# Kernel tuning notes

Measured on AMD Instinct MI355X. Metric: run time of the kernel, lower is better.

## Reference

```python
import jax, jax.numpy as jnp
import numpy as np

D = 1024        # d_model
H = 16          # n_heads
DF = 4096       # d_ff
MAXL = 1024     # max_len
MAXSTEPS = 24   # max_steps


def setup_inputs() -> dict:
    key = jax.random.key(0)
    ks = jax.random.split(key, 10)
    B, S = 4, 1024
    s = 0.02
    f32 = jnp.float32
    return {
        "x": jax.random.normal(ks[0], (B, S, D), f32),
        "original_input": jax.random.normal(ks[1], (B, S, D), f32),
        "think_step": 5,
        "step_embed": jax.random.normal(ks[2], (MAXSTEPS, D), f32) * s,
        "Wqkv": jax.random.normal(ks[3], (D, 3 * D), f32) * s,
        "bqkv": jnp.zeros((3 * D,), f32),
        "Wout": jax.random.normal(ks[4], (D, D), f32) * s,
        "bout": jnp.zeros((D,), f32),
        "Wg": jax.random.normal(ks[5], (2 * D, D), f32) * s,
        "bg": jnp.zeros((D,), f32),
        "rel_pos_bias": jax.random.normal(ks[6], (2 * MAXL - 1,), f32) * s,
        "W1": jax.random.normal(ks[7], (D, DF), f32) * s,
        "b1": jnp.zeros((DF,), f32),
        "W2": jax.random.normal(ks[8], (DF, D), f32) * s,
        "b2": jnp.zeros((D,), f32),
        "ln1_g": jnp.ones((D,), f32),
        "ln1_b": jnp.zeros((D,), f32),
        "ln2_g": jnp.ones((D,), f32),
        "ln2_b": jnp.zeros((D,), f32),
    }


def _layer_norm(x, g, b, eps=1e-5):
    m = jnp.mean(x, axis=-1, keepdims=True)
    v = jnp.mean((x - m) ** 2, axis=-1, keepdims=True)
    return (x - m) * jax.lax.rsqrt(v + eps) * g + b


def reference(x, original_input, think_step, step_embed, Wqkv, bqkv, Wout, bout,
              Wg, bg, rel_pos_bias, W1, b1, W2, b2, ln1_g, ln1_b, ln2_g, ln2_b):
    B, S, _ = x.shape
    hd = D // H
    # gated residual input injection
    gate = jax.nn.sigmoid(jnp.concatenate([x, original_input], axis=-1) @ Wg + bg)
    x = x * (1.0 - gate) + original_input * gate
    # think-step embedding (clamped)
    step = min(int(think_step), MAXSTEPS - 1)
    x = x + step_embed[step][None, None, :]
    # qkv projection -> (3, B, H, S, hd)
    qkv = (x @ Wqkv + bqkv).reshape(B, S, 3, H, hd).transpose(2, 0, 3, 1, 4)
    q, k, v = qkv[0], qkv[1], qkv[2]
    scores = jnp.einsum('bhqd,bhkd->bhqk', q, k) * (hd ** -0.5)
    # relative position bias: dist clamped to [0, 2*MAXL-2]
    pos = jnp.arange(S)
    rel = jnp.clip(pos[:, None] - pos[None, :] + (MAXL - 1), 0, 2 * MAXL - 2)
    scores = scores + rel_pos_bias[rel][None, None]  # (B,H,S,S)
    probs = jax.nn.softmax(scores, axis=-1)
    attn = jnp.einsum('bhqk,bhkd->bhqd', probs, v)
    attn = attn.transpose(0, 2, 1, 3).reshape(B, S, D)
    attn = attn @ Wout + bout
    x = _layer_norm(x + attn, ln1_g, ln1_b)
    h = jax.nn.gelu(x @ W1 + b1, approximate=False) @ W2 + b2
    return _layer_norm(x + h, ln2_g, ln2_b)
```

## Files before the change

kernel.cpp:

```cpp
#include <hip/hip_runtime.h>
#include <hip/hip_bf16.h>
#include <math.h>

#define D_MODEL 1024
#define NH      16
#define HD      64
#define DFF     4096
#define SEQ     1024
#define BATCH   4
#define TOK     (BATCH*SEQ)
#define MAXSTEPS 24

typedef __hip_bfloat16 bf16;
typedef __attribute__((ext_vector_type(8))) short short8;
typedef __attribute__((ext_vector_type(4))) float floatx4;

__device__ __forceinline__ float b2f(bf16 v){ return __bfloat162float(v); }
__device__ __forceinline__ bf16  f2b(float v){ return __float2bfloat16(v); }

__device__ __forceinline__ void gload_lds16(const bf16* g, bf16* l){
    __builtin_amdgcn_global_load_lds((const __attribute__((address_space(1))) void*)g,
                                     (__attribute__((address_space(3))) void*)l, 16, 0, 0);
}

template<int TN, int EPI, bool SPLITK>
__global__ __launch_bounds__(256)
void mfma_gemm(const bf16* __restrict__ A, const bf16* __restrict__ Bt,
               const float* __restrict__ bias, void* __restrict__ outv,
               void* __restrict__ outv2,
               int M, int N, int K, int lda, int ldb,
               const float* __restrict__ xg, const float* __restrict__ og,
               const float* __restrict__ seg, const int* __restrict__ stepp)
{
    constexpr int NT  = TN / 32;
    constexpr int NBP = TN / 64;
    constexpr int R   = (TN == 64) ? 4 : 3;
    __shared__ bf16 As[R][128 * 32];
    __shared__ bf16 Bs[R][TN * 32];
    const int tid  = threadIdx.x;
    const int lane = tid & 63;
    const int w    = tid >> 6;
    const int wm   = w & 1, wn = w >> 1;
    const int fr   = lane & 15;
    const int q    = lane >> 4;

    if (SPLITK) {
        int z = blockIdx.z;
        A  += (size_t)z * K;
        Bt += (size_t)z * K;
    }

    const int tn_g = gridDim.x;
    const int nwg  = tn_g * gridDim.y;
    const int bid  = blockIdx.y * tn_g + blockIdx.x;
    const int o    = (bid & 7) * (nwg >> 3) + (bid >> 3);
    const int bandw = 8 * tn_g;
    const int band  = o / bandw;
    const int rr    = o - band * bandw;
    const int row0 = (band * 8 + (rr & 7)) * 128;
    const int col0 = (rr >> 3) * TN;

    const bf16* gA[2]; int sA_[2];
    #pragma unroll
    for (int p = 0; p < 2; ++p) {
        int s  = p * 256 + tid;
        int m  = s >> 2;
        int qg = (s & 3) ^ ((m >> 1) & 3);
        gA[p]  = A + (size_t)(row0 + m) * lda + qg * 8;
        sA_[p] = s * 8;
    }
    const bf16* gB[NBP]; int sB_[NBP];
    #pragma unroll
    for (int p = 0; p < NBP; ++p) {
        int s  = p * 256 + tid;
        int m  = s >> 2;
        int qg = (s & 3) ^ ((m >> 1) & 3);
        gB[p]  = Bt + (size_t)(col0 + m) * ldb + qg * 8;
        sB_[p] = s * 8;
    }

    int aoff[4], boff[NT];
    #pragma unroll
    for (int t = 0; t < 4; ++t) {
        int ml  = wm * 64 + t * 16 + fr;
        aoff[t] = (ml * 4 + (q ^ ((ml >> 1) & 3))) * 8;
    }
    #pragma unroll
    for (int t = 0; t < NT; ++t) {
        int nl  = wn * (TN / 2) + t * 16 + fr;
        boff[t] = (nl * 4 + (q ^ ((nl >> 1) & 3))) * 8;
    }

    #pragma unroll
    for (int pt = 0; pt < R - 1; ++pt) {
        #pragma unroll
        for (int p = 0; p < 2; ++p)   gload_lds16(gA[p] + pt * 32, &As[pt][sA_[p]]);
        #pragma unroll
        for (int p = 0; p < NBP; ++p) gload_lds16(gB[p] + pt * 32, &Bs[pt][sB_[p]]);
    }

    floatx4 acc[4][NT] = {};
    const int nk = K >> 5;
    int cur = 0;
    int kst = (R - 1) * 32;

    for (int t = 0; t < nk; ++t) {
        if constexpr (TN == 64) asm volatile("s_waitcnt vmcnt(6)" ::: "memory");
        else                    asm volatile("s_waitcnt vmcnt(4)" ::: "memory");
        __builtin_amdgcn_s_barrier();
        asm volatile("" ::: "memory");

        if (kst < K) {
            int sb = (cur == 0) ? (R - 1) : (cur - 1);
            #pragma unroll
            for (int p = 0; p < 2; ++p)   gload_lds16(gA[p] + kst, &As[sb][sA_[p]]);
            #pragma unroll
            for (int p = 0; p < NBP; ++p) gload_lds16(gB[p] + kst, &Bs[sb][sB_[p]]);
            kst += 32;
        }

        short8 af[4], bfg[NT];
        #pragma unroll
        for (int i = 0; i < 4; ++i)  af[i]  = *(const short8*)(&As[cur][aoff[i]]);
        #pragma unroll
        for (int j = 0; j < NT; ++j) bfg[j] = *(const short8*)(&Bs[cur][boff[j]]);
        #pragma unroll
        for (int i = 0; i < 4; ++i)
            #pragma unroll
            for (int j = 0; j < NT; ++j)
                acc[i][j] = __builtin_amdgcn_mfma_f32_16x16x32_bf16(af[i], bfg[j], acc[i][j], 0, 0, 0);

        cur = (cur == R - 1) ? 0 : (cur + 1);
    }

    void* outp = outv;
    float bscale = 1.0f;
    if (SPLITK && blockIdx.z != 0) { outp = outv2; bscale = 0.0f; }

    int st = 0;
    if (EPI == 3) {
        st = stepp[0];
        st = st < 0 ? 0 : (st > MAXSTEPS - 1 ? MAXSTEPS - 1 : st);
    }

    float bv[NT], sv[NT];
    #pragma unroll
    for (int nt = 0; nt < NT; ++nt) {
        int col = col0 + wn * (TN / 2) + nt * 16 + fr;
        bv[nt] = bias[col] * bscale;
        if (EPI == 3) sv[nt] = seg[st * D_MODEL + col];
    }
    #pragma unroll
    for (int mt = 0; mt < 4; ++mt) {
        #pragma unroll
        for (int nt = 0; nt < NT; ++nt) {
            int col = col0 + wn * (TN / 2) + nt * 16 + fr;
            #pragma unroll
            for (int r = 0; r < 4; ++r) {
                int row = row0 + wm * 64 + mt * 16 + q * 4 + r;
                float v = acc[mt][nt][r] + bv[nt];
                if (EPI == 0) {
                    ((float*)outp)[(size_t)row * N + col] = v;
                } else if (EPI == 1) {
                    ((bf16*)outp)[(size_t)row * N + col] = f2b(v);
                } else {
                    float g = 1.0f / (1.0f + __expf(-v));
                    size_t idx = (size_t)row * N + col;
                    float mix = xg[idx] * (1.0f - g) + og[idx] * g + sv[nt];
                    ((bf16*)outp)[idx] = f2b(mix);
                }
            }
        }
    }
}

template<int EPI>
__global__ __launch_bounds__(256, 2)
void gemm_wide(const bf16* __restrict__ A, const bf16* __restrict__ Bt,
               const float* __restrict__ bias, bf16* __restrict__ out,
               int M, int N, int K)
{
    constexpr int R = 3;
    __shared__ bf16 As[R][256 * 32];
    __shared__ bf16 Bs[R][128 * 32];
    const int tid  = threadIdx.x;
    const int lane = tid & 63;
    const int w    = tid >> 6;
    const int wm   = w & 1, wn = w >> 1;
    const int fr   = lane & 15;
    const int q    = lane >> 4;

    const int tn_g = gridDim.x;
    const int nwg  = tn_g * gridDim.y;
    const int bid  = blockIdx.y * tn_g + blockIdx.x;
    const int o    = (bid & 7) * (nwg >> 3) + (bid >> 3);
    const int bandw = 8 * tn_g;
    const int band  = o / bandw;
    const int rr    = o - band * bandw;
    const int row0 = (band * 8 + (rr & 7)) * 256;
    const int col0 = (rr >> 3) * 128;

    const bf16* gA[4]; int sA_[4];
    #pragma unroll
    for (int p = 0; p < 4; ++p) {
        int s  = p * 256 + tid;
        int m  = s >> 2;
        int qg = (s & 3) ^ ((m >> 1) & 3);
        gA[p]  = A + (size_t)(row0 + m) * K + qg * 8;
        sA_[p] = s * 8;
    }
    const bf16* gB[2]; int sB_[2];
    #pragma unroll
    for (int p = 0; p < 2; ++p) {
        int s  = p * 256 + tid;
        int m  = s >> 2;
        int qg = (s & 3) ^ ((m >> 1) & 3);
        gB[p]  = Bt + (size_t)(col0 + m) * K + qg * 8;
        sB_[p] = s * 8;
    }

    int aoff[8], boff[4];
    #pragma unroll
    for (int t = 0; t < 8; ++t) {
        int ml  = wm * 128 + t * 16 + fr;
        aoff[t] = (ml * 4 + (q ^ ((ml >> 1) & 3))) * 8;
    }
    #pragma unroll
    for (int t = 0; t < 4; ++t) {
        int nl  = wn * 64 + t * 16 + fr;
        boff[t] = (nl * 4 + (q ^ ((nl >> 1) & 3))) * 8;
    }

    #pragma unroll
    for (int pt = 0; pt < R - 1; ++pt) {
        #pragma unroll
        for (int p = 0; p < 4; ++p) gload_lds16(gA[p] + pt * 32, &As[pt][sA_[p]]);
        #pragma unroll
        for (int p = 0; p < 2; ++p) gload_lds16(gB[p] + pt * 32, &Bs[pt][sB_[p]]);
    }

    floatx4 acc[8][4] = {};
    const int nk = K >> 5;
    int cur = 0;
    int kst = (R - 1) * 32;

    for (int t = 0; t < nk; ++t) {
        asm volatile("s_waitcnt vmcnt(6)" ::: "memory");
        __builtin_amdgcn_s_barrier();
        asm volatile("" ::: "memory");

        if (kst < K) {
            int sb = (cur == 0) ? (R - 1) : (cur - 1);
            #pragma unroll
            for (int p = 0; p < 4; ++p) gload_lds16(gA[p] + kst, &As[sb][sA_[p]]);
            #pragma unroll
            for (int p = 0; p < 2; ++p) gload_lds16(gB[p] + kst, &Bs[sb][sB_[p]]);
            kst += 32;
        }

        short8 af[8], bfg[4];
        #pragma unroll
        for (int i = 0; i < 8; ++i) af[i]  = *(const short8*)(&As[cur][aoff[i]]);
        #pragma unroll
        for (int j = 0; j < 4; ++j) bfg[j] = *(const short8*)(&Bs[cur][boff[j]]);
        __builtin_amdgcn_s_setprio(1);
        #pragma unroll
        for (int i = 0; i < 8; ++i)
            #pragma unroll
            for (int j = 0; j < 4; ++j)
                acc[i][j] = __builtin_amdgcn_mfma_f32_16x16x32_bf16(af[i], bfg[j], acc[i][j], 0, 0, 0);
        __builtin_amdgcn_s_setprio(0);

        cur = (cur == R - 1) ? 0 : (cur + 1);
    }

    float bv[4];
    #pragma unroll
    for (int j = 0; j < 4; ++j) bv[j] = bias[col0 + wn * 64 + j * 16 + fr];
    #pragma unroll
    for (int mt = 0; mt < 8; ++mt) {
        #pragma unroll
        for (int nt = 0; nt < 4; ++nt) {
            int col = col0 + wn * 64 + nt * 16 + fr;
            #pragma unroll
            for (int r = 0; r < 4; ++r) {
                int row = row0 + wm * 128 + mt * 16 + q * 4 + r;
                float v = acc[mt][nt][r] + bv[nt];
                if (EPI == 1) {
                    out[(size_t)row * N + col] = f2b(v);
                } else {
                    float g = 0.5f * v * (1.0f + erff(v * 0.70710678118654752f));
                    out[(size_t)row * N + col] = f2b(g);
                }
            }
        }
    }
}

#define NTRANS_BLOCKS 14336
__global__ __launch_bounds__(256)
void transpose_all_kernel(const float* __restrict__ Wg,   bf16* __restrict__ WgT,
                          const float* __restrict__ Wqkv, bf16* __restrict__ WqkvT,
                          const float* __restrict__ Wout, bf16* __restrict__ WoutT,
                          const float* __restrict__ W1,   bf16* __restrict__ W1T,
                          const float* __restrict__ W2,   bf16* __restrict__ W2T)
{
    __shared__ float t[32][33];
    const int bid = blockIdx.x;
    if (bid >= NTRANS_BLOCKS) return;
    const float* W; bf16* WT; int K, N, base;
    if      (bid <  2048) { W = Wg;   WT = WgT;   K = 2048; N = 1024; base = 0; }
    else if (bid <  5120) { W = Wqkv; WT = WqkvT; K = 1024; N = 3072; base = 2048; }
    else if (bid <  6144) { W = Wout; WT = WoutT; K = 1024; N = 1024; base = 5120; }
    else if (bid < 10240) { W = W1;   WT = W1T;   K = 1024; N = 4096; base = 6144; }
    else                  { W = W2;   WT = W2T;   K = 4096; N = 1024; base = 10240; }
    const int lb  = bid - base;
    const int ntx = N >> 5;
    const int n0 = (lb % ntx) * 32, k0 = (lb / ntx) * 32;
    const int tx = threadIdx.x & 31, ty = threadIdx.x >> 5;
    #pragma unroll
    for (int i = 0; i < 4; ++i)
        t[ty + i * 8][tx] = W[(size_t)(k0 + ty + i * 8) * N + n0 + tx];
    __syncthreads();
    #pragma unroll
    for (int i = 0; i < 4; ++i)
        WT[(size_t)(n0 + ty + i * 8) * K + k0 + tx] = f2b(t[tx][ty + i * 8]);
}

__global__ __launch_bounds__(256)
void xcat_kernel(const float* __restrict__ x, const float* __restrict__ orig,
                 bf16* __restrict__ xcat)
{
    int i = blockIdx.x * 256 + threadIdx.x;
    float4 xv = ((const float4*)x)[i];
    float4 ov = ((const float4*)orig)[i];
    int t = i >> 8, c4 = (i & 255) * 4;
    bf16* px = xcat + (size_t)t * 2048 + c4;
    px[0] = f2b(xv.x); px[1] = f2b(xv.y); px[2] = f2b(xv.z); px[3] = f2b(xv.w);
    bf16* po = px + 1024;
    po[0] = f2b(ov.x); po[1] = f2b(ov.y); po[2] = f2b(ov.z); po[3] = f2b(ov.w);
}

__global__ __launch_bounds__(256)
void vtrans_kernel(const bf16* __restrict__ qkv, bf16* __restrict__ Vt)
{
    __shared__ float t[32][33];
    const int blk = blockIdx.x;
    const int dt = blk & 1;
    const int st = (blk >> 1) & 31;
    const int h  = (blk >> 6) & 15;
    const int b  = blk >> 10;
    const int tx = threadIdx.x & 31, ty = threadIdx.x >> 5;
    #pragma unroll
    for (int i = 0; i < 4; ++i)
        t[ty + i * 8][tx] = b2f(qkv[(size_t)(b * SEQ + st * 32 + ty + i * 8) * 3072
                                    + 2048 + h * 64 + dt * 32 + tx]);
    __syncthreads();
    #pragma unroll
    for (int i = 0; i < 4; ++i)
        Vt[(size_t)((b * NH + h) * 64 + dt * 32 + ty + i * 8) * SEQ + st * 32 + tx]
            = f2b(t[tx][ty + i * 8]);
}

__global__ __launch_bounds__(256)
void fattn_kernel(const bf16* __restrict__ qkv, const bf16* __restrict__ Vt,
                  const float* __restrict__ relb, bf16* __restrict__ out)
{
    __shared__ bf16 KPs[128 * 64];
    __shared__ bf16 Vs [64 * 128];
    __shared__ float relb_s[1088];

    const int tid  = threadIdx.x;
    const int lane = tid & 63;
    const int w    = tid >> 6;
    const int fr   = lane & 15;
    const int quad = lane >> 4;

    const int qt = blockIdx.x & 15;
    const int h  = (blockIdx.x >> 4) & 15;
    const int b  = blockIdx.x >> 8;
    const int bq = b * SEQ;
    const int bh = b * NH + h;

    for (int i = tid; i < 1087; i += 256)
        relb_s[i] = relb[qt * 64 + i] - 8.0f;

    const int qrow = bq + qt * 64 + w * 16 + fr;
    short8 qf[2];
    {
        const bf16* qp = qkv + (size_t)qrow * 3072 + h * 64 + quad * 8;
        qf[0] = *(const short8*)(qp);
        qf[1] = *(const short8*)(qp + 32);
    }

    int ibase[4];
    #pragma unroll
    for (int r = 0; r < 4; ++r)
        ibase[r] = (w * 16 + quad * 4 + r) - fr + 1023;

    float lsum[4] = {0.f, 0.f, 0.f, 0.f};
    floatx4 accO[4];
    #pragma unroll
    for (int nt = 0; nt < 4; ++nt) accO[nt] = (floatx4){0.f, 0.f, 0.f, 0.f};

    for (int k0 = 0; k0 < SEQ; k0 += 128) {
        __syncthreads();
        #pragma unroll
        for (int it = 0; it < 4; ++it) {
            int s = it * 256 + tid;
            int key = s >> 3, cs = s & 7;
            int c = cs ^ (key & 7);
            const bf16* src = qkv + (size_t)(bq + k0 + key) * 3072 + 1024 + h * 64 + c * 8;
            gload_lds16(src, KPs + (size_t)s * 8);
        }
        #pragma unroll
        for (int it = 0; it < 4; ++it) {
            int s = it * 256 + tid;
            int row = s >> 4, cs = s & 15;
            int c = cs ^ (row & 15);
            const bf16* src = Vt + (size_t)(bh * 64 + row) * SEQ + k0 + c * 8;
            gload_lds16(src, Vs + (size_t)s * 8);
        }
        __syncthreads();

        floatx4 accS[8];
        #pragma unroll
        for (int t = 0; t < 8; ++t) accS[t] = (floatx4){0.f, 0.f, 0.f, 0.f};
        __builtin_amdgcn_s_setprio(1);
        #pragma unroll
        for (int t = 0; t < 8; ++t) {
            int row = t * 16 + fr;
            #pragma unroll
            for (int ks = 0; ks < 2; ++ks) {
                int slot = (ks * 4 + quad) ^ (row & 7);
                short8 kf = *(const short8*)(KPs + (size_t)row * 64 + slot * 8);
                accS[t] = __builtin_amdgcn_mfma_f32_16x16x32_bf16(qf[ks], kf, accS[t], 0, 0, 0);
            }
        }
        __builtin_amdgcn_s_setprio(0);

        __syncthreads();

        bf16* Ps = KPs + w * 2048;
        #pragma unroll
        for (int t = 0; t < 8; ++t) {
            int keyl = t * 16 + fr;
            int cbase = keyl >> 3, koff = keyl & 7;
            #pragma unroll
            for (int r = 0; r < 4; ++r) {
                float bias = relb_s[ibase[r] - k0 - t * 16];
                float p = __expf(fmaf(accS[t][r], 0.125f, bias));
                lsum[r] += p;
                int row = quad * 4 + r;
                int slot = cbase ^ (row & 15);
                Ps[(size_t)row * 128 + slot * 8 + koff] = f2b(p);
            }
        }

        __builtin_amdgcn_s_setprio(1);
        #pragma unroll
        for (int ks = 0; ks < 4; ++ks) {
            int slotp = (ks * 4 + quad) ^ (fr & 15);
            short8 pf = *(const short8*)(Ps + (size_t)fr * 128 + slotp * 8);
            #pragma unroll
            for (int nt = 0; nt < 4; ++nt) {
                int vrow = nt * 16 + fr;
                int slotv = (ks * 4 + quad) ^ (vrow & 15);
                short8 vf = *(const short8*)(Vs + (size_t)vrow * 128 + slotv * 8);
                accO[nt] = __builtin_amdgcn_mfma_f32_16x16x32_bf16(pf, vf, accO[nt], 0, 0, 0);
            }
        }
        __builtin_amdgcn_s_setprio(0);
    }

    float inv[4];
    #pragma unroll
    for (int r = 0; r < 4; ++r) {
        float v = lsum[r];
        v += __shfl_xor(v, 1); v += __shfl_xor(v, 2);
        v += __shfl_xor(v, 4); v += __shfl_xor(v, 8);
        inv[r] = 1.0f / v;
    }

    #pragma unroll
    for (int nt = 0; nt < 4; ++nt) {
        int col = h * 64 + nt * 16 + fr;
        #pragma unroll
        for (int r = 0; r < 4; ++r) {
            int t = bq + qt * 64 + w * 16 + quad * 4 + r;
            out[(size_t)t * D_MODEL + col] = f2b(accO[nt][r] * inv[r]);
        }
    }
}

template<bool OUT_BF16, bool HAS2>
__global__ __launch_bounds__(256)
void ln_kernel(const bf16* __restrict__ a, const float* __restrict__ add,
               const float* __restrict__ add2,
               const float* __restrict__ g, const float* __restrict__ bb,
               void* __restrict__ outv)
{
    __shared__ float red[256];
    __shared__ float red2[256];
    const int row = blockIdx.x;
    const int tid = threadIdx.x;
    float s[4];
    float lsum = 0.f, lsq = 0.f;
    #pragma unroll
    for (int u = 0; u < 4; ++u) {
        int i = tid + 256 * u;
        float v = b2f(a[row * D_MODEL + i]) + add[row * D_MODEL + i];
        if (HAS2) v += add2[row * D_MODEL + i];
        s[u] = v; lsum += v; lsq += v * v;
    }
    red[tid] = lsum; red2[tid] = lsq; __syncthreads();
    for (int s2 = 128; s2 > 0; s2 >>= 1) {
        if (tid < s2) { red[tid] += red[tid + s2]; red2[tid] += red2[tid + s2]; }
        __syncthreads();
    }
    float mean = red[0] * (1.0f / D_MODEL);
    float var  = red2[0] * (1.0f / D_MODEL) - mean * mean;
    float rs = rsqrtf(var + 1e-5f);
    #pragma unroll
    for (int u = 0; u < 4; ++u) {
        int i = tid + 256 * u;
        float o = (s[u] - mean) * rs * g[i] + bb[i];
        if (OUT_BF16) ((bf16*)outv)[row * D_MODEL + i] = f2b(o);
        else          ((float*)outv)[row * D_MODEL + i] = o;
    }
}

extern "C" void kernel_launch(void* const* d_in, const int* in_sizes, int n_in,
                              void* d_out, int out_size, void* d_ws, size_t ws_size,
                              hipStream_t stream)
{
    const float* x     = (const float*)d_in[0];
    const float* orig  = (const float*)d_in[1];
    const int*   step  = (const int*)  d_in[2];
    const float* se    = (const float*)d_in[3];
    const float* Wqkv  = (const float*)d_in[4];
    const float* bqkv  = (const float*)d_in[5];
    const float* Wout  = (const float*)d_in[6];
    const float* bout  = (const float*)d_in[7];
    const float* Wg    = (const float*)d_in[8];
    const float* bg    = (const float*)d_in[9];
    const float* relb  = (const float*)d_in[10];
    const float* W1    = (const float*)d_in[11];
    const float* b1    = (const float*)d_in[12];
    const float* W2    = (const float*)d_in[13];
    const float* b2    = (const float*)d_in[14];
    const float* ln1g  = (const float*)d_in[15];
    const float* ln1b  = (const float*)d_in[16];
    const float* ln2g  = (const float*)d_in[17];
    const float* ln2b  = (const float*)d_in[18];

    char* ws = (char*)d_ws;
    bf16* WgT   = (bf16*)(ws);
    bf16* WqkvT = (bf16*)(ws + ( 4u << 20));
    bf16* WoutT = (bf16*)(ws + (10u << 20));
    bf16* W1T   = (bf16*)(ws + (12u << 20));
    bf16* W2T   = (bf16*)(ws + (20u << 20));
    bf16* xw    = (bf16*)(ws + (28u << 20));
    bf16* xcat  = (bf16*)(ws + (36u << 20));
    bf16* attnb = (bf16*)(ws + (36u << 20));
    bf16* h     = (bf16*)(ws + (44u << 20));
    bf16* qkvb  = (bf16*)(ws + (52u << 20));
    float* tmp2 = (float*)(ws);
    bf16* Vt    = (bf16*)d_out;
    float* tmp  = (float*)d_out;

    dim3 blk(256);

    transpose_all_kernel<<<NTRANS_BLOCKS, blk, 0, stream>>>(Wg, WgT, Wqkv, WqkvT,
                                                    Wout, WoutT, W1, W1T, W2, W2T);
    xcat_kernel<<<TOK, blk, 0, stream>>>(x, orig, xcat);

    mfma_gemm<64, 3, false><<<dim3(D_MODEL/64, TOK/128), blk, 0, stream>>>(
        xcat, WgT, bg, xw, nullptr, TOK, D_MODEL, 2*D_MODEL, 2*D_MODEL, 2*D_MODEL,
        x, orig, se, step);

    gemm_wide<1><<<dim3(3*D_MODEL/128, TOK/256), blk, 0, stream>>>(
        xw, WqkvT, bqkv, qkvb, TOK, 3*D_MODEL, D_MODEL);

    vtrans_kernel<<<BATCH*NH*64, blk, 0, stream>>>(qkvb, Vt);

    fattn_kernel<<<BATCH*NH*(SEQ/64), blk, 0, stream>>>(qkvb, Vt, relb, attnb);

    mfma_gemm<64, 0, false><<<dim3(D_MODEL/64, TOK/128), blk, 0, stream>>>(
        attnb, WoutT, bout, tmp, nullptr, TOK, D_MODEL, D_MODEL, D_MODEL, D_MODEL,
        nullptr, nullptr, nullptr, nullptr);

    ln_kernel<true, false><<<TOK, blk, 0, stream>>>(xw, tmp, nullptr, ln1g, ln1b, xw);

    gemm_wide<2><<<dim3(DFF/128, TOK/256), blk, 0, stream>>>(
        xw, W1T, b1, h, TOK, DFF, D_MODEL);

    mfma_gemm<128, 0, true><<<dim3(D_MODEL/128, TOK/128, 2), blk, 0, stream>>>(
        h, W2T, b2, tmp, tmp2, TOK, D_MODEL, DFF/2, DFF, DFF,
        nullptr, nullptr, nullptr, nullptr);

    ln_kernel<false, true><<<TOK, blk, 0, stream>>>(xw, tmp, tmp2, ln2g, ln2b, d_out);
}
```

Measured before the change: 432.0 us.

## Load A fragments directly into registers in wide GEMM, keep B in LDS

The wide GEMM used for QKV and FFN1 no longer stages the A tile through LDS. Each wave loads its A fragments straight from global memory into registers, double-buffered across two k-steps, while B stays in a triple-buffered LDS ring. This cuts LDS traffic and footprint and removes the A LDS reads. In exchange, A is fetched redundantly by the waves that share a row block, and register pressure rises, with global-load latency exposed more directly to the MFMA loop.

```diff
diff --git a/kernel.cpp b/kernel.cpp
--- a/kernel.cpp
+++ b/kernel.cpp
@@ -176,13 +176,11 @@
 
 template<int EPI>
 __global__ __launch_bounds__(256, 2)
-void gemm_wide(const bf16* __restrict__ A, const bf16* __restrict__ Bt,
+void gemm_areg(const bf16* __restrict__ A, const bf16* __restrict__ Bt,
                const float* __restrict__ bias, bf16* __restrict__ out,
                int M, int N, int K)
 {
-    constexpr int R = 3;
-    __shared__ bf16 As[R][256 * 32];
-    __shared__ bf16 Bs[R][128 * 32];
+    __shared__ bf16 Bs[3][128 * 32];
     const int tid  = threadIdx.x;
     const int lane = tid & 63;
     const int w    = tid >> 6;
@@ -200,15 +198,11 @@
     const int row0 = (band * 8 + (rr & 7)) * 256;
     const int col0 = (rr >> 3) * 128;
 
-    const bf16* gA[4]; int sA_[4];
-    #pragma unroll
-    for (int p = 0; p < 4; ++p) {
-        int s  = p * 256 + tid;
-        int m  = s >> 2;
-        int qg = (s & 3) ^ ((m >> 1) & 3);
-        gA[p]  = A + (size_t)(row0 + m) * K + qg * 8;
-        sA_[p] = s * 8;
-    }
+    const bf16* gAf[8];
+    #pragma unroll
+    for (int i = 0; i < 8; ++i)
+        gAf[i] = A + (size_t)(row0 + wm * 128 + i * 16 + fr) * K + q * 8;
+
     const bf16* gB[2]; int sB_[2];
     #pragma unroll
     for (int p = 0; p < 2; ++p) {
@@ -218,61 +212,82 @@
         gB[p]  = Bt + (size_t)(col0 + m) * K + qg * 8;
         sB_[p] = s * 8;
     }
-
-    int aoff[8], boff[4];
-    #pragma unroll
-    for (int t = 0; t < 8; ++t) {
-        int ml  = wm * 128 + t * 16 + fr;
-        aoff[t] = (ml * 4 + (q ^ ((ml >> 1) & 3))) * 8;
-    }
+    int boff[4];
     #pragma unroll
     for (int t = 0; t < 4; ++t) {
         int nl  = wn * 64 + t * 16 + fr;
         boff[t] = (nl * 4 + (q ^ ((nl >> 1) & 3))) * 8;
     }
 
-    #pragma unroll
-    for (int pt = 0; pt < R - 1; ++pt) {
-        #pragma unroll
-        for (int p = 0; p < 4; ++p) gload_lds16(gA[p] + pt * 32, &As[pt][sA_[p]]);
-        #pragma unroll
-        for (int p = 0; p < 2; ++p) gload_lds16(gB[p] + pt * 32, &Bs[pt][sB_[p]]);
-    }
+#define STAGE_B(TAU, BUF)                                                     \
+    { _Pragma("unroll")                                                       \
+      for (int p = 0; p < 2; ++p)                                             \
+          gload_lds16(gB[p] + (TAU) * 32, &Bs[BUF][sB_[p]]); }
+
+    short8 af0[8], af1[8];
+
+    #pragma unroll
+    for (int i = 0; i < 8; ++i) af0[i] = *(const short8*)(gAf[i]);
+    STAGE_B(0, 0);
+    STAGE_B(1, 1);
+    asm volatile("s_waitcnt vmcnt(2)" ::: "memory");
+    __builtin_amdgcn_s_barrier();
+    asm volatile("" ::: "memory");
 
     floatx4 acc[8][4] = {};
     const int nk = K >> 5;
-    int cur = 0;
-    int kst = (R - 1) * 32;
-
-    for (int t = 0; t < nk; ++t) {
-        asm volatile("s_waitcnt vmcnt(6)" ::: "memory");
+    int bcur = 0;
+
+    for (int t = 0; t < nk; t += 2) {
+        int bn1 = (bcur == 2) ? 0 : bcur + 1;
+        int bn2 = (bn1  == 2) ? 0 : bn1 + 1;
+        if (t + 1 < nk) {
+            int k1 = (t + 1) << 5;
+            #pragma unroll
+            for (int i = 0; i < 8; ++i) af1[i] = *(const short8*)(gAf[i] + k1);
+        }
+        if (t + 2 < nk) STAGE_B(t + 2, bn2);
+        {
+            short8 bfg[4];
+            #pragma unroll
+            for (int j = 0; j < 4; ++j) bfg[j] = *(const short8*)(&Bs[bcur][boff[j]]);
+            __builtin_amdgcn_s_setprio(1);
+            #pragma unroll
+            for (int i = 0; i < 8; ++i)
+                #pragma unroll
+                for (int j = 0; j < 4; ++j)
+                    acc[i][j] = __builtin_amdgcn_mfma_f32_16x16x32_bf16(af0[i], bfg[j], acc[i][j], 0, 0, 0);
+            __builtin_amdgcn_s_setprio(0);
+        }
+        asm volatile("s_waitcnt vmcnt(2)" ::: "memory");
         __builtin_amdgcn_s_barrier();
         asm volatile("" ::: "memory");
 
-        if (kst < K) {
-            int sb = (cur == 0) ? (R - 1) : (cur - 1);
-            #pragma unroll
-            for (int p = 0; p < 4; ++p) gload_lds16(gA[p] + kst, &As[sb][sA_[p]]);
-            #pragma unroll
-            for (int p = 0; p < 2; ++p) gload_lds16(gB[p] + kst, &Bs[sb][sB_[p]]);
-            kst += 32;
-        }
-
-        short8 af[8], bfg[4];
-        #pragma unroll
-        for (int i = 0; i < 8; ++i) af[i]  = *(const short8*)(&As[cur][aoff[i]]);
-        #pragma unroll
-        for (int j = 0; j < 4; ++j) bfg[j] = *(const short8*)(&Bs[cur][boff[j]]);
-        __builtin_amdgcn_s_setprio(1);
-        #pragma unroll
-        for (int i = 0; i < 8; ++i)
-            #pragma unroll
-            for (int j = 0; j < 4; ++j)
-                acc[i][j] = __builtin_amdgcn_mfma_f32_16x16x32_bf16(af[i], bfg[j], acc[i][j], 0, 0, 0);
-        __builtin_amdgcn_s_setprio(0);
-
-        cur = (cur == R - 1) ? 0 : (cur + 1);
-    }
+        if (t + 2 < nk) {
+            int k2 = (t + 2) << 5;
+            #pragma unroll
+            for (int i = 0; i < 8; ++i) af0[i] = *(const short8*)(gAf[i] + k2);
+        }
+        if (t + 3 < nk) STAGE_B(t + 3, bcur);
+        {
+            short8 bfg[4];
+            #pragma unroll
+            for (int j = 0; j < 4; ++j) bfg[j] = *(const short8*)(&Bs[bn1][boff[j]]);
+            __builtin_amdgcn_s_setprio(1);
+            #pragma unroll
+            for (int i = 0; i < 8; ++i)
+                #pragma unroll
+                for (int j = 0; j < 4; ++j)
+                    acc[i][j] = __builtin_amdgcn_mfma_f32_16x16x32_bf16(af1[i], bfg[j], acc[i][j], 0, 0, 0);
+            __builtin_amdgcn_s_setprio(0);
+        }
+        asm volatile("s_waitcnt vmcnt(2)" ::: "memory");
+        __builtin_amdgcn_s_barrier();
+        asm volatile("" ::: "memory");
+
+        bcur = bn2;
+    }
+#undef STAGE_B
 
     float bv[4];
     #pragma unroll
@@ -579,7 +594,7 @@
         xcat, WgT, bg, xw, nullptr, TOK, D_MODEL, 2*D_MODEL, 2*D_MODEL, 2*D_MODEL,
         x, orig, se, step);
 
-    gemm_wide<1><<<dim3(3*D_MODEL/128, TOK/256), blk, 0, stream>>>(
+    gemm_areg<1><<<dim3(3*D_MODEL/128, TOK/256), blk, 0, stream>>>(
         xw, WqkvT, bqkv, qkvb, TOK, 3*D_MODEL, D_MODEL);
 
     vtrans_kernel<<<BATCH*NH*64, blk, 0, stream>>>(qkvb, Vt);
@@ -592,7 +607,7 @@
 
     ln_kernel<true, false><<<TOK, blk, 0, stream>>>(xw, tmp, nullptr, ln1g, ln1b, xw);
 
-    gemm_wide<2><<<dim3(DFF/128, TOK/256), blk, 0, stream>>>(
+    gemm_areg<2><<<dim3(DFF/128, TOK/256), blk, 0, stream>>>(
         xw, W1T, b1, h, TOK, DFF, D_MODEL);
 
     mfma_gemm<128, 0, true><<<dim3(D_MODEL/128, TOK/128, 2), blk, 0, stream>>>(
```

Result: slower. 492.7 us (+14.0%).

## Process 32 query rows per wave in flash attention with dedicated P buffer

Applied to the files above, without the earlier changes.

Each attention block now covers 128 queries, each wave handling two 16-row groups, so every K/V tile staged in LDS is reused by twice as many queries and the grid is halved. P is written to its own LDS region instead of aliasing the K buffer, which removes the barrier between the QK^T MFMAs and the softmax write. This raises LDS and register use per block, which may lower occupancy and leave fewer blocks to fill the GPU.

```diff
diff --git a/kernel.cpp b/kernel.cpp
--- a/kernel.cpp
+++ b/kernel.cpp
@@ -368,7 +368,8 @@
 {
     __shared__ bf16 KPs[128 * 64];
     __shared__ bf16 Vs [64 * 128];
-    __shared__ float relb_s[1088];
+    __shared__ bf16 Ps [4 * 32 * 128];
+    __shared__ float relb_s[1152];
 
     const int tid  = threadIdx.x;
     const int lane = tid & 63;
@@ -376,32 +377,39 @@
     const int fr   = lane & 15;
     const int quad = lane >> 4;
 
-    const int qt = blockIdx.x & 15;
-    const int h  = (blockIdx.x >> 4) & 15;
-    const int b  = blockIdx.x >> 8;
+    const int qt = blockIdx.x & 7;
+    const int h  = (blockIdx.x >> 3) & 15;
+    const int b  = blockIdx.x >> 7;
     const int bq = b * SEQ;
     const int bh = b * NH + h;
 
-    for (int i = tid; i < 1087; i += 256)
-        relb_s[i] = relb[qt * 64 + i] - 8.0f;
-
-    const int qrow = bq + qt * 64 + w * 16 + fr;
-    short8 qf[2];
-    {
-        const bf16* qp = qkv + (size_t)qrow * 3072 + h * 64 + quad * 8;
-        qf[0] = *(const short8*)(qp);
-        qf[1] = *(const short8*)(qp + 32);
-    }
-
-    int ibase[4];
-    #pragma unroll
-    for (int r = 0; r < 4; ++r)
-        ibase[r] = (w * 16 + quad * 4 + r) - fr + 1023;
-
-    float lsum[4] = {0.f, 0.f, 0.f, 0.f};
-    floatx4 accO[4];
-    #pragma unroll
-    for (int nt = 0; nt < 4; ++nt) accO[nt] = (floatx4){0.f, 0.f, 0.f, 0.f};
+    for (int i = tid; i < 1151; i += 256)
+        relb_s[i] = relb[qt * 128 + i] - 8.0f;
+
+    short8 qf[2][2];
+    #pragma unroll
+    for (int g = 0; g < 2; ++g) {
+        const bf16* qp = qkv + (size_t)(bq + qt * 128 + w * 32 + g * 16 + fr) * 3072
+                         + h * 64 + quad * 8;
+        qf[g][0] = *(const short8*)(qp);
+        qf[g][1] = *(const short8*)(qp + 32);
+    }
+
+    int ibase[2][4];
+    #pragma unroll
+    for (int g = 0; g < 2; ++g)
+        #pragma unroll
+        for (int r = 0; r < 4; ++r)
+            ibase[g][r] = (w * 32 + g * 16 + quad * 4 + r) - fr + 1023;
+
+    float lsum[2][4] = {};
+    floatx4 accO[2][4];
+    #pragma unroll
+    for (int g = 0; g < 2; ++g)
+        #pragma unroll
+        for (int nt = 0; nt < 4; ++nt) accO[g][nt] = (floatx4){0.f, 0.f, 0.f, 0.f};
+
+    bf16* Pw = Ps + w * (32 * 128);
 
     for (int k0 = 0; k0 < SEQ; k0 += 128) {
         __syncthreads();
@@ -423,37 +431,37 @@
         }
         __syncthreads();
 
-        floatx4 accS[8];
-        #pragma unroll
-        for (int t = 0; t < 8; ++t) accS[t] = (floatx4){0.f, 0.f, 0.f, 0.f};
-        __builtin_amdgcn_s_setprio(1);
-        #pragma unroll
-        for (int t = 0; t < 8; ++t) {
-            int row = t * 16 + fr;
-            #pragma unroll
-            for (int ks = 0; ks < 2; ++ks) {
-                int slot = (ks * 4 + quad) ^ (row & 7);
-                short8 kf = *(const short8*)(KPs + (size_t)row * 64 + slot * 8);
-                accS[t] = __builtin_amdgcn_mfma_f32_16x16x32_bf16(qf[ks], kf, accS[t], 0, 0, 0);
+        #pragma unroll
+        for (int g = 0; g < 2; ++g) {
+            floatx4 accS[8];
+            #pragma unroll
+            for (int t = 0; t < 8; ++t) accS[t] = (floatx4){0.f, 0.f, 0.f, 0.f};
+            __builtin_amdgcn_s_setprio(1);
+            #pragma unroll
+            for (int t = 0; t < 8; ++t) {
+                int row = t * 16 + fr;
+                #pragma unroll
+                for (int ks = 0; ks < 2; ++ks) {
+                    int slot = (ks * 4 + quad) ^ (row & 7);
+                    short8 kf = *(const short8*)(KPs + (size_t)row * 64 + slot * 8);
+                    accS[t] = __builtin_amdgcn_mfma_f32_16x16x32_bf16(qf[g][ks], kf, accS[t], 0, 0, 0);
+                }
             }
-        }
-        __builtin_amdgcn_s_setprio(0);
-
-        __syncthreads();
-
-        bf16* Ps = KPs + w * 2048;
-        #pragma unroll
-        for (int t = 0; t < 8; ++t) {
-            int keyl = t * 16 + fr;
-            int cbase = keyl >> 3, koff = keyl & 7;
-            #pragma unroll
-            for (int r = 0; r < 4; ++r) {
-                float bias = relb_s[ibase[r] - k0 - t * 16];
-                float p = __expf(fmaf(accS[t][r], 0.125f, bias));
-                lsum[r] += p;
-                int row = quad * 4 + r;
-                int slot = cbase ^ (row & 15);
-                Ps[(size_t)row * 128 + slot * 8 + koff] = f2b(p);
+            __builtin_amdgcn_s_setprio(0);
+
+            #pragma unroll
+            for (int t = 0; t < 8; ++t) {
+                int keyl = t * 16 + fr;
+                int cbase = keyl >> 3, koff = keyl & 7;
+                #pragma unroll
+                for (int r = 0; r < 4; ++r) {
+                    float bias = relb_s[ibase[g][r] - k0 - t * 16];
+                    float p = __expf(fmaf(accS[t][r], 0.125f, bias));
+                    lsum[g][r] += p;
+                    int row = g * 16 + quad * 4 + r;
+                    int slot = cbase ^ (row & 15);
+                    Pw[(size_t)row * 128 + slot * 8 + koff] = f2b(p);
+                }
             }
         }
 
@@ -461,36 +469,42 @@
         #pragma unroll
         for (int ks = 0; ks < 4; ++ks) {
             int slotp = (ks * 4 + quad) ^ (fr & 15);
-            short8 pf = *(const short8*)(Ps + (size_t)fr * 128 + slotp * 8);
+            short8 pf0 = *(const short8*)(Pw + (size_t)fr * 128 + slotp * 8);
+            short8 pf1 = *(const short8*)(Pw + (size_t)(16 + fr) * 128 + slotp * 8);
             #pragma unroll
             for (int nt = 0; nt < 4; ++nt) {
                 int vrow = nt * 16 + fr;
                 int slotv = (ks * 4 + quad) ^ (vrow & 15);
                 short8 vf = *(const short8*)(Vs + (size_t)vrow * 128 + slotv * 8);
-                accO[nt] = __builtin_amdgcn_mfma_f32_16x16x32_bf16(pf, vf, accO[nt], 0, 0, 0);
+                accO[0][nt] = __builtin_amdgcn_mfma_f32_16x16x32_bf16(pf0, vf, accO[0][nt], 0, 0, 0);
+                accO[1][nt] = __builtin_amdgcn_mfma_f32_16x16x32_bf16(pf1, vf, accO[1][nt], 0, 0, 0);
             }
         }
         __builtin_amdgcn_s_setprio(0);
     }
 
-    float inv[4];
-    #pragma unroll
-    for (int r = 0; r < 4; ++r) {
-        float v = lsum[r];
-        v += __shfl_xor(v, 1); v += __shfl_xor(v, 2);
-        v += __shfl_xor(v, 4); v += __shfl_xor(v, 8);
-        inv[r] = 1.0f / v;
-    }
-
-    #pragma unroll
-    for (int nt = 0; nt < 4; ++nt) {
-        int col = h * 64 + nt * 16 + fr;
+    float inv[2][4];
+    #pragma unroll
+    for (int g = 0; g < 2; ++g)
         #pragma unroll
         for (int r = 0; r < 4; ++r) {
-            int t = bq + qt * 64 + w * 16 + quad * 4 + r;
-            out[(size_t)t * D_MODEL + col] = f2b(accO[nt][r] * inv[r]);
-        }
-    }
+            float v = lsum[g][r];
+            v += __shfl_xor(v, 1); v += __shfl_xor(v, 2);
+            v += __shfl_xor(v, 4); v += __shfl_xor(v, 8);
+            inv[g][r] = 1.0f / v;
+        }
+
+    #pragma unroll
+    for (int g = 0; g < 2; ++g)
+        #pragma unroll
+        for (int nt = 0; nt < 4; ++nt) {
+            int col = h * 64 + nt * 16 + fr;
+            #pragma unroll
+            for (int r = 0; r < 4; ++r) {
+                int t = bq + qt * 128 + w * 32 + g * 16 + quad * 4 + r;
+                out[(size_t)t * D_MODEL + col] = f2b(accO[g][nt][r] * inv[g][r]);
+            }
+        }
 }
 
 template<bool OUT_BF16, bool HAS2>
@@ -584,7 +598,7 @@
 
     vtrans_kernel<<<BATCH*NH*64, blk, 0, stream>>>(qkvb, Vt);
 
-    fattn_kernel<<<BATCH*NH*(SEQ/64), blk, 0, stream>>>(qkvb, Vt, relb, attnb);
+    fattn_kernel<<<BATCH*NH*(SEQ/128), blk, 0, stream>>>(qkvb, Vt, relb, attnb);
 
     mfma_gemm<64, 0, false><<<dim3(D_MODEL/64, TOK/128), blk, 0, stream>>>(
         attnb, WoutT, bout, tmp, nullptr, TOK, D_MODEL, D_MODEL, D_MODEL, D_MODEL,
```

Result: no change. 428.3 us (-0.8%).
